# Optimization experiments

Hardware: AMD Instinct MI355X
Metric: run time of the kernel (lower is better)

## Reference

```python
import jax, jax.numpy as jnp
import numpy as np

N_ATOMS = 200000
N_FEAT = 1024
N_SPECIES = 4
N_STRUCT = 2000
OUT = 1
H1, H2 = 256, 256
SCALE = 1.0  # energies_scale_factor


def setup_inputs() -> dict:
    key = jax.random.key(0)
    ks = jax.random.split(key, 8)
    ps = jax.random.normal(ks[0], (N_ATOMS, N_FEAT), dtype=jnp.float32)
    numbers = jax.random.randint(ks[1], (N_ATOMS,), 0, N_SPECIES, dtype=jnp.int32)
    batch = jnp.sort(jax.random.randint(ks[2], (N_ATOMS,), 0, N_STRUCT, dtype=jnp.int32))
    # learned params (all Linear layers are bias-free in the source)
    W_comp = jax.random.normal(ks[3], (OUT, N_SPECIES), dtype=jnp.float32) * 0.1
    W_psl = jax.random.normal(ks[4], (OUT, N_FEAT), dtype=jnp.float32) * (N_FEAT ** -0.5)
    W_h1 = jax.random.normal(ks[5], (H1, N_FEAT), dtype=jnp.float32) * (N_FEAT ** -0.5)
    W_h2 = jax.random.normal(ks[6], (H2, H1), dtype=jnp.float32) * (H1 ** -0.5)
    W_out = jax.random.normal(ks[7], (OUT, H2), dtype=jnp.float32) * (H2 ** -0.5)
    return {"ps": ps, "numbers": numbers, "batch": batch,
            "W_comp": W_comp, "W_psl": W_psl, "W_h1": W_h1, "W_h2": W_h2, "W_out": W_out}


def reference(ps, numbers, batch, W_comp, W_psl, W_h1, W_h2, W_out):
    # compositions: per-structure counts of each species -> [S, n_species]
    one_hot = jax.nn.one_hot(numbers, N_SPECIES, dtype=ps.dtype)
    compositions = jax.ops.segment_sum(one_hot, batch, num_segments=N_STRUCT)
    energies = compositions @ W_comp.T  # [S, OUT]

    # linear branch: per-atom linear then index_add_ (segment sum) over structures
    psl = ps @ W_psl.T  # [N, OUT]
    energies_psl = jax.ops.segment_sum(psl, batch, num_segments=N_STRUCT)

    # MLP branch: Linear+SiLU stack, final Linear, then segment sum
    h = jax.nn.silu(ps @ W_h1.T)
    h = jax.nn.silu(h @ W_h2.T)
    psnn = h @ W_out.T  # [N, OUT]
    energies_psnn = jax.ops.segment_sum(psnn, batch, num_segments=N_STRUCT)

    return energies + (energies_psl + energies_psnn) * SCALE
```

## Files before the change

kernel.cpp:

```cpp
#include <hip/hip_runtime.h>
#include <cstdint>

#define N_ATOMS 200000
#define N_FEAT  1024
#define HDIM    256
#define N_STRUCT 2000
#define M_TILE  64
#define SCALE   1.0f

typedef __bf16 bf16x8 __attribute__((ext_vector_type(8)));
typedef float  f32x4  __attribute__((ext_vector_type(4)));

__device__ __forceinline__ void gl_lds16(const void* g, void* l) {
    __builtin_amdgcn_global_load_lds(
        (const __attribute__((address_space(1))) uint32_t*)g,
        (__attribute__((address_space(3))) uint32_t*)l, 16, 0, 0);
}

__global__ void convert_w(const float* __restrict__ W1, const float* __restrict__ W2,
                          __bf16* __restrict__ w1b, __bf16* __restrict__ w2b) {
    int i = blockIdx.x * 256 + threadIdx.x;
    if (i < 262144) w1b[i] = (__bf16)W1[i];
    int j = i - 262144;
    if (j >= 0 && j < 65536) w2b[j] = (__bf16)W2[j];
}

__global__ __launch_bounds__(256, 2) void fused_mlp(
    const float* __restrict__ ps, const int* __restrict__ numbers, const int* __restrict__ batch,
    const float* __restrict__ W_comp, const float* __restrict__ W_psl, const float* __restrict__ W_out,
    const __bf16* __restrict__ w1b, const __bf16* __restrict__ w2b,
    float* __restrict__ out)
{
    __shared__ __align__(16) __bf16 A1[M_TILE * 32];
    __shared__ __align__(16) __bf16 Bb[HDIM * 32];
    __shared__ __align__(16) __bf16 A2[M_TILE * 264];
    __shared__ float evec[M_TILE];

    const int t    = threadIdx.x;
    const int wave = t >> 6;
    const int lane = t & 63;
    const int quad = lane >> 4;
    const int l15  = lane & 15;
    const int atom0 = blockIdx.x * M_TILE;

    const int r_a  = t >> 2;
    const int ks_a = (t & 3) * 8;
    const float* psrow = ps + (size_t)(atom0 + r_a) * N_FEAT + ks_a;

    f32x4 acc[4][4];
#pragma unroll
    for (int i = 0; i < 4; ++i)
#pragma unroll
        for (int j = 0; j < 4; ++j) acc[i][j] = (f32x4){0.f, 0.f, 0.f, 0.f};

    float psl_acc = 0.f;

    for (int k0 = 0; k0 < N_FEAT; k0 += 32) {
        float4 f0 = *(const float4*)(psrow + k0);
        float4 f1 = *(const float4*)(psrow + k0 + 4);
        float4 w0 = *(const float4*)(W_psl + k0 + ks_a);
        float4 w1 = *(const float4*)(W_psl + k0 + ks_a + 4);
        psl_acc += f0.x * w0.x + f0.y * w0.y + f0.z * w0.z + f0.w * w0.w
                 + f1.x * w1.x + f1.y * w1.y + f1.z * w1.z + f1.w * w1.w;
        bf16x8 av;
        av[0] = (__bf16)f0.x; av[1] = (__bf16)f0.y; av[2] = (__bf16)f0.z; av[3] = (__bf16)f0.w;
        av[4] = (__bf16)f1.x; av[5] = (__bf16)f1.y; av[6] = (__bf16)f1.z; av[7] = (__bf16)f1.w;
        *(bf16x8*)&A1[t * 8] = av;

#pragma unroll
        for (int p = 0; p < 4; ++p) {
            const __bf16* gsrc = w1b + (size_t)(p * 64 + r_a) * N_FEAT + k0 + ks_a;
            gl_lds16(gsrc, &Bb[p * 2048 + t * 8]);
        }
        __syncthreads();

        bf16x8 afrag[4];
#pragma unroll
        for (int mt = 0; mt < 4; ++mt)
            afrag[mt] = *(const bf16x8*)&A1[(mt * 16 + l15) * 32 + quad * 8];
#pragma unroll
        for (int nt = 0; nt < 4; ++nt) {
            int n = wave * 64 + nt * 16 + l15;
            bf16x8 bfrag = *(const bf16x8*)&Bb[n * 32 + quad * 8];
#pragma unroll
            for (int mt = 0; mt < 4; ++mt)
                acc[mt][nt] = __builtin_amdgcn_mfma_f32_16x16x32_bf16(afrag[mt], bfrag, acc[mt][nt], 0, 0, 0);
        }
        __syncthreads();
    }

    psl_acc += __shfl_xor(psl_acc, 1);
    psl_acc += __shfl_xor(psl_acc, 2);
    if ((t & 3) == 0) evec[r_a] = psl_acc;

#pragma unroll
    for (int mt = 0; mt < 4; ++mt)
#pragma unroll
        for (int nt = 0; nt < 4; ++nt) {
            int n = wave * 64 + nt * 16 + l15;
#pragma unroll
            for (int rg = 0; rg < 4; ++rg) {
                float x = acc[mt][nt][rg];
                float s = x / (1.f + __expf(-x));
                A2[(mt * 16 + quad * 4 + rg) * 264 + n] = (__bf16)s;
                acc[mt][nt][rg] = 0.f;
            }
        }
    __syncthreads();

    for (int k0 = 0; k0 < HDIM; k0 += 32) {
#pragma unroll
        for (int p = 0; p < 4; ++p) {
            const __bf16* gsrc = w2b + (size_t)(p * 64 + r_a) * HDIM + k0 + ks_a;
            gl_lds16(gsrc, &Bb[p * 2048 + t * 8]);
        }
        __syncthreads();
        bf16x8 afrag[4];
#pragma unroll
        for (int mt = 0; mt < 4; ++mt)
            afrag[mt] = *(const bf16x8*)&A2[(mt * 16 + l15) * 264 + k0 + quad * 8];
#pragma unroll
        for (int nt = 0; nt < 4; ++nt) {
            int n = wave * 64 + nt * 16 + l15;
            bf16x8 bfrag = *(const bf16x8*)&Bb[n * 32 + quad * 8];
#pragma unroll
            for (int mt = 0; mt < 4; ++mt)
                acc[mt][nt] = __builtin_amdgcn_mfma_f32_16x16x32_bf16(afrag[mt], bfrag, acc[mt][nt], 0, 0, 0);
        }
        __syncthreads();
    }

    float pr[4][4];
#pragma unroll
    for (int mt = 0; mt < 4; ++mt)
#pragma unroll
        for (int rg = 0; rg < 4; ++rg) pr[mt][rg] = 0.f;

#pragma unroll
    for (int nt = 0; nt < 4; ++nt) {
        int n = wave * 64 + nt * 16 + l15;
        float wv = W_out[n];
#pragma unroll
        for (int mt = 0; mt < 4; ++mt)
#pragma unroll
            for (int rg = 0; rg < 4; ++rg) {
                float x = acc[mt][nt][rg];
                pr[mt][rg] += (x / (1.f + __expf(-x))) * wv;
            }
    }
#pragma unroll
    for (int mask = 1; mask <= 8; mask <<= 1)
#pragma unroll
        for (int mt = 0; mt < 4; ++mt)
#pragma unroll
            for (int rg = 0; rg < 4; ++rg)
                pr[mt][rg] += __shfl_xor(pr[mt][rg], mask);
    if (l15 == 0) {
#pragma unroll
        for (int mt = 0; mt < 4; ++mt)
#pragma unroll
            for (int rg = 0; rg < 4; ++rg)
                atomicAdd(&evec[mt * 16 + quad * 4 + rg], pr[mt][rg]);
    }
    __syncthreads();

    if (t < M_TILE) {
        int atom = atom0 + t;
        int b = batch[atom];
        float e = W_comp[numbers[atom]] + SCALE * evec[t];
#pragma unroll
        for (int d = 1; d < 64; d <<= 1) {
            float vu = __shfl_up(e, d);
            int   bu = __shfl_up(b, d);
            if (lane >= d && bu == b) e += vu;
        }
        int bn = __shfl_down(b, 1);
        if (lane == 63 || bn != b) atomicAdd(&out[b], e);
    }
}

extern "C" void kernel_launch(void* const* d_in, const int* in_sizes, int n_in,
                              void* d_out, int out_size, void* d_ws, size_t ws_size,
                              hipStream_t stream) {
    const float* ps     = (const float*)d_in[0];
    const int*   numbers= (const int*)d_in[1];
    const int*   batch  = (const int*)d_in[2];
    const float* W_comp = (const float*)d_in[3];
    const float* W_psl  = (const float*)d_in[4];
    const float* W_h1   = (const float*)d_in[5];
    const float* W_h2   = (const float*)d_in[6];
    const float* W_out  = (const float*)d_in[7];
    float* out = (float*)d_out;

    __bf16* w1b = (__bf16*)d_ws;
    __bf16* w2b = w1b + 262144;

    hipMemsetAsync(d_out, 0, (size_t)out_size * sizeof(float), stream);
    convert_w<<<1280, 256, 0, stream>>>(W_h1, W_h2, w1b, w2b);
    fused_mlp<<<3125, 256, 0, stream>>>(ps, numbers, batch, W_comp, W_psl, W_out, w1b, w2b, out);
}
```

Baseline: 1.246 ms.

## Double-buffer LDS tiles, prefetch ps registers, and swizzle LDS layouts

Both GEMM loops now double-buffer their LDS tiles. The next weight tile is issued via global_load_lds, and the next ps tile is held in registers, while MFMAs run on the current buffer. This cuts the two barriers per k-step to one. The A1 tile is padded to a stride of 40 and the B tile gets an XOR swizzle on its k-chunk to reduce LDS bank conflicts. LDS use roughly doubles for A1/Bb, which may affect the two-blocks-per-CU occupancy target, and register pressure rises from the prefetched float4s.

Result: faster. 1.207 ms (-3.2%).

```diff
diff --git a/kernel.cpp b/kernel.cpp
--- a/kernel.cpp
+++ b/kernel.cpp
@@ -7,6 +7,7 @@
 #define N_STRUCT 2000
 #define M_TILE  64
 #define SCALE   1.0f
+#define A1_LD   40
 
 typedef __bf16 bf16x8 __attribute__((ext_vector_type(8)));
 typedef float  f32x4  __attribute__((ext_vector_type(4)));
@@ -16,6 +17,8 @@
         (const __attribute__((address_space(1))) uint32_t*)g,
         (__attribute__((address_space(3))) uint32_t*)l, 16, 0, 0);
 }
+
+__device__ __forceinline__ float silu(float x) { return x / (1.f + __expf(-x)); }
 
 __global__ void convert_w(const float* __restrict__ W1, const float* __restrict__ W2,
                           __bf16* __restrict__ w1b, __bf16* __restrict__ w2b) {
@@ -31,8 +34,8 @@
     const __bf16* __restrict__ w1b, const __bf16* __restrict__ w2b,
     float* __restrict__ out)
 {
-    __shared__ __align__(16) __bf16 A1[M_TILE * 32];
-    __shared__ __align__(16) __bf16 Bb[HDIM * 32];
+    __shared__ __align__(16) __bf16 A1[2][M_TILE * A1_LD];
+    __shared__ __align__(16) __bf16 Bb[2][HDIM * 32];
     __shared__ __align__(16) __bf16 A2[M_TILE * 264];
     __shared__ float evec[M_TILE];
 
@@ -43,9 +46,13 @@
     const int l15  = lane & 15;
     const int atom0 = blockIdx.x * M_TILE;
 
-    const int r_a  = t >> 2;
-    const int ks_a = (t & 3) * 8;
-    const float* psrow = ps + (size_t)(atom0 + r_a) * N_FEAT + ks_a;
+    const int r_a = t >> 2;
+    const int c_a = t & 3;
+    const int s_a = c_a ^ ((t >> 3) & 3);
+    const int bq  = quad ^ ((l15 >> 1) & 3);
+
+    const float* psrow = ps + (size_t)(atom0 + r_a) * N_FEAT + c_a * 8;
+    const float* wpsl  = W_psl + c_a * 8;
 
     f32x4 acc[4][4];
 #pragma unroll
@@ -55,77 +62,111 @@
 
     float psl_acc = 0.f;
 
-    for (int k0 = 0; k0 < N_FEAT; k0 += 32) {
-        float4 f0 = *(const float4*)(psrow + k0);
-        float4 f1 = *(const float4*)(psrow + k0 + 4);
-        float4 w0 = *(const float4*)(W_psl + k0 + ks_a);
-        float4 w1 = *(const float4*)(W_psl + k0 + ks_a + 4);
+    int a1_off[4], b_off[4];
+#pragma unroll
+    for (int mt = 0; mt < 4; ++mt) a1_off[mt] = (mt * 16 + l15) * A1_LD + quad * 8;
+#pragma unroll
+    for (int nt = 0; nt < 4; ++nt) b_off[nt] = (wave * 64 + nt * 16 + l15) * 32 + bq * 8;
+
+    {
+        float4 f0 = *(const float4*)(psrow);
+        float4 f1 = *(const float4*)(psrow + 4);
+        float4 w0 = *(const float4*)(wpsl);
+        float4 w1 = *(const float4*)(wpsl + 4);
         psl_acc += f0.x * w0.x + f0.y * w0.y + f0.z * w0.z + f0.w * w0.w
                  + f1.x * w1.x + f1.y * w1.y + f1.z * w1.z + f1.w * w1.w;
         bf16x8 av;
         av[0] = (__bf16)f0.x; av[1] = (__bf16)f0.y; av[2] = (__bf16)f0.z; av[3] = (__bf16)f0.w;
         av[4] = (__bf16)f1.x; av[5] = (__bf16)f1.y; av[6] = (__bf16)f1.z; av[7] = (__bf16)f1.w;
-        *(bf16x8*)&A1[t * 8] = av;
-
-#pragma unroll
-        for (int p = 0; p < 4; ++p) {
-            const __bf16* gsrc = w1b + (size_t)(p * 64 + r_a) * N_FEAT + k0 + ks_a;
-            gl_lds16(gsrc, &Bb[p * 2048 + t * 8]);
+        *(bf16x8*)&A1[0][r_a * A1_LD + c_a * 8] = av;
+#pragma unroll
+        for (int p = 0; p < 4; ++p)
+            gl_lds16(w1b + (size_t)(p * 64 + r_a) * N_FEAT + s_a * 8, &Bb[0][p * 2048 + t * 8]);
+    }
+    float4 g0 = *(const float4*)(psrow + 32);
+    float4 g1 = *(const float4*)(psrow + 36);
+    float4 x0 = *(const float4*)(wpsl + 32);
+    float4 x1 = *(const float4*)(wpsl + 36);
+    __syncthreads();
+
+    for (int i = 0; i < 32; ++i) {
+        const int cur = i & 1;
+        if (i < 31) {
+            const int k1 = (i + 1) * 32;
+#pragma unroll
+            for (int p = 0; p < 4; ++p)
+                gl_lds16(w1b + (size_t)(p * 64 + r_a) * N_FEAT + k1 + s_a * 8,
+                         &Bb[cur ^ 1][p * 2048 + t * 8]);
+        }
+        bf16x8 af[4];
+#pragma unroll
+        for (int mt = 0; mt < 4; ++mt) af[mt] = *(const bf16x8*)&A1[cur][a1_off[mt]];
+#pragma unroll
+        for (int nt = 0; nt < 4; ++nt) {
+            bf16x8 bf_ = *(const bf16x8*)&Bb[cur][b_off[nt]];
+#pragma unroll
+            for (int mt = 0; mt < 4; ++mt)
+                acc[mt][nt] = __builtin_amdgcn_mfma_f32_16x16x32_bf16(af[mt], bf_, acc[mt][nt], 0, 0, 0);
+        }
+        if (i < 31) {
+            psl_acc += g0.x * x0.x + g0.y * x0.y + g0.z * x0.z + g0.w * x0.w
+                     + g1.x * x1.x + g1.y * x1.y + g1.z * x1.z + g1.w * x1.w;
+            bf16x8 av;
+            av[0] = (__bf16)g0.x; av[1] = (__bf16)g0.y; av[2] = (__bf16)g0.z; av[3] = (__bf16)g0.w;
+            av[4] = (__bf16)g1.x; av[5] = (__bf16)g1.y; av[6] = (__bf16)g1.z; av[7] = (__bf16)g1.w;
+            *(bf16x8*)&A1[cur ^ 1][r_a * A1_LD + c_a * 8] = av;
+            if (i < 30) {
+                const int k2 = (i + 2) * 32;
+                g0 = *(const float4*)(psrow + k2);
+                g1 = *(const float4*)(psrow + k2 + 4);
+                x0 = *(const float4*)(wpsl + k2);
+                x1 = *(const float4*)(wpsl + k2 + 4);
+            }
         }
         __syncthreads();
-
-        bf16x8 afrag[4];
-#pragma unroll
-        for (int mt = 0; mt < 4; ++mt)
-            afrag[mt] = *(const bf16x8*)&A1[(mt * 16 + l15) * 32 + quad * 8];
+    }
+
+    psl_acc += __shfl_xor(psl_acc, 1);
+    psl_acc += __shfl_xor(psl_acc, 2);
+    if (c_a == 0) evec[r_a] = psl_acc;
+
+#pragma unroll
+    for (int mt = 0; mt < 4; ++mt)
 #pragma unroll
         for (int nt = 0; nt < 4; ++nt) {
             int n = wave * 64 + nt * 16 + l15;
-            bf16x8 bfrag = *(const bf16x8*)&Bb[n * 32 + quad * 8];
-#pragma unroll
-            for (int mt = 0; mt < 4; ++mt)
-                acc[mt][nt] = __builtin_amdgcn_mfma_f32_16x16x32_bf16(afrag[mt], bfrag, acc[mt][nt], 0, 0, 0);
-        }
-        __syncthreads();
-    }
-
-    psl_acc += __shfl_xor(psl_acc, 1);
-    psl_acc += __shfl_xor(psl_acc, 2);
-    if ((t & 3) == 0) evec[r_a] = psl_acc;
-
-#pragma unroll
-    for (int mt = 0; mt < 4; ++mt)
-#pragma unroll
-        for (int nt = 0; nt < 4; ++nt) {
-            int n = wave * 64 + nt * 16 + l15;
 #pragma unroll
             for (int rg = 0; rg < 4; ++rg) {
                 float x = acc[mt][nt][rg];
-                float s = x / (1.f + __expf(-x));
-                A2[(mt * 16 + quad * 4 + rg) * 264 + n] = (__bf16)s;
+                A2[(mt * 16 + quad * 4 + rg) * 264 + n] = (__bf16)silu(x);
                 acc[mt][nt][rg] = 0.f;
             }
         }
+#pragma unroll
+    for (int p = 0; p < 4; ++p)
+        gl_lds16(w2b + (size_t)(p * 64 + r_a) * HDIM + s_a * 8, &Bb[0][p * 2048 + t * 8]);
     __syncthreads();
 
-    for (int k0 = 0; k0 < HDIM; k0 += 32) {
-#pragma unroll
-        for (int p = 0; p < 4; ++p) {
-            const __bf16* gsrc = w2b + (size_t)(p * 64 + r_a) * HDIM + k0 + ks_a;
-            gl_lds16(gsrc, &Bb[p * 2048 + t * 8]);
-        }
-        __syncthreads();
-        bf16x8 afrag[4];
-#pragma unroll
-        for (int mt = 0; mt < 4; ++mt)
-            afrag[mt] = *(const bf16x8*)&A2[(mt * 16 + l15) * 264 + k0 + quad * 8];
+    for (int i = 0; i < 8; ++i) {
+        const int cur = i & 1;
+        if (i < 7) {
+            const int k1 = (i + 1) * 32;
+#pragma unroll
+            for (int p = 0; p < 4; ++p)
+                gl_lds16(w2b + (size_t)(p * 64 + r_a) * HDIM + k1 + s_a * 8,
+                         &Bb[cur ^ 1][p * 2048 + t * 8]);
+        }
+        const int k0 = i * 32;
+        bf16x8 af[4];
+#pragma unroll
+        for (int mt = 0; mt < 4; ++mt)
+            af[mt] = *(const bf16x8*)&A2[(mt * 16 + l15) * 264 + k0 + quad * 8];
 #pragma unroll
         for (int nt = 0; nt < 4; ++nt) {
-            int n = wave * 64 + nt * 16 + l15;
-            bf16x8 bfrag = *(const bf16x8*)&Bb[n * 32 + quad * 8];
+            bf16x8 bf_ = *(const bf16x8*)&Bb[cur][b_off[nt]];
 #pragma unroll
             for (int mt = 0; mt < 4; ++mt)
-                acc[mt][nt] = __builtin_amdgcn_mfma_f32_16x16x32_bf16(afrag[mt], bfrag, acc[mt][nt], 0, 0, 0);
+                acc[mt][nt] = __builtin_amdgcn_mfma_f32_16x16x32_bf16(af[mt], bf_, acc[mt][nt], 0, 0, 0);
         }
         __syncthreads();
     }
@@ -145,7 +186,7 @@
 #pragma unroll
             for (int rg = 0; rg < 4; ++rg) {
                 float x = acc[mt][nt][rg];
-                pr[mt][rg] += (x / (1.f + __expf(-x))) * wv;
+                pr[mt][rg] += silu(x) * wv;
             }
     }
 #pragma unroll
```
